# Kernel optimization log

Measured on AMD Instinct MI355X. Metric: run time of the kernel, lower is better.

The kernel has to match this reference:

```python
import jax, jax.numpy as jnp
import numpy as np

N = 20000      # base graph nodes
S = 20         # nodes per subgraph
NC = N * S     # combined subgraph nodes = 400000
EC = 2_000_000 # combined subgraph edges
EB = 200_000   # base graph edges
NIN = 64
HOP = 16
D = NIN + HOP  # 80, conv width
NOUT = 64


def setup_inputs() -> dict:
    key = jax.random.key(0)
    ks = jax.random.split(key, 32)
    f32 = jnp.float32

    batch = jnp.repeat(jnp.arange(N), S)                      # subgraph id per combined node
    offs = jax.random.randint(ks[0], (NC,), 1, N)
    nodes_mapper = (batch + offs) % N                         # never equals batch
    cent_idx = jnp.arange(N) * S
    nodes_mapper = nodes_mapper.at[cent_idx].set(jnp.arange(N))  # exactly one centroid/subgraph

    edge_index = jax.random.randint(ks[1], (2, EC), 0, NC)
    edges_mapper = jax.random.randint(ks[2], (EC,), 0, EB)
    hop_indicator = jax.random.randint(ks[3], (NC,), 0, 19)   # +1 -> [1,19] < 20

    x = jax.random.normal(ks[4], (N, NIN), f32)
    edge_attr = jax.random.normal(ks[5], (EB, D), f32)

    def lin(k, i, o, s=0.05):
        return jax.random.normal(k, (i, o), f32) * s

    inp = dict(
        x=x, edge_attr=edge_attr,
        hop_table=jax.random.normal(ks[6], (20, HOP), f32) * 0.05,
        conv_w1=lin(ks[7], D, D), bn1_g=jnp.ones((D,), f32), bn1_b=jnp.zeros((D,), f32),
        conv_w2=lin(ks[8], D, D), bn2_g=jnp.ones((D,), f32), bn2_b=jnp.zeros((D,), f32),
        oe_w=lin(ks[9], D, NOUT), oe_b=jnp.zeros((NOUT,), f32),
        sub_w=lin(ks[10], NOUT, NOUT), sub_b=jnp.zeros((NOUT,), f32),
        sub_g=jnp.ones((NOUT,), f32), sub_bt=jnp.zeros((NOUT,), f32),
        ctx_w=lin(ks[11], NOUT, NOUT), ctx_b=jnp.zeros((NOUT,), f32),
        ctx_g=jnp.ones((NOUT,), f32), ctx_bt=jnp.zeros((NOUT,), f32),
        gc_w=lin(ks[12], HOP, NOUT), gc_b=jnp.zeros((NOUT,), f32),
        gs_w=lin(ks[13], HOP, NOUT), gs_b=jnp.zeros((NOUT,), f32),
        gx_w=lin(ks[14], HOP, NOUT), gx_b=jnp.zeros((NOUT,), f32),
        fo_w=lin(ks[15], NOUT, NOUT), fo_b=jnp.zeros((NOUT,), f32),
        fo_g=jnp.ones((NOUT,), f32), fo_bt=jnp.zeros((NOUT,), f32),
        nodes_mapper=nodes_mapper, edges_mapper=edges_mapper,
        edge_index=edge_index, batch=batch, hop_indicator=hop_indicator,
    )
    return inp


def reference(x, edge_attr, hop_table,
              conv_w1, bn1_g, bn1_b, conv_w2, bn2_g, bn2_b, oe_w, oe_b,
              sub_w, sub_b, sub_g, sub_bt, ctx_w, ctx_b, ctx_g, ctx_bt,
              gc_w, gc_b, gs_w, gs_b, gx_w, gx_b,
              fo_w, fo_b, fo_g, fo_bt,
              nodes_mapper, edges_mapper, edge_index, batch, hop_indicator):
    hop_emb = hop_table[hop_indicator + 1]                       # [NC, HOP]
    h = jnp.concatenate([x[nodes_mapper], hop_emb], axis=-1)     # [NC, D] gather + concat
    ea = edge_attr[edges_mapper]                                 # [EC, D] gather
    src, dst = edge_index[0], edge_index[1]

    def gine_layer(h, W, g, b):
        # GINEConv (eps=0, no bias): Linear(x_i + sum_j ReLU(x_j + e_ji)), then eval-BN + ReLU
        msg = jax.nn.relu(h[src] + ea)                           # [EC, D]
        agg = jax.ops.segment_sum(msg, dst, num_segments=NC)     # scatter-add
        out = (h + agg) @ W
        return jax.nn.relu(g * out + b)

    prev = h
    h = gine_layer(h, conv_w1, bn1_g, bn1_b) + prev
    prev = h
    h = gine_layer(h, conv_w2, bn2_g, bn2_b) + prev
    comb = h @ oe_w + oe_b                                       # [NC, NOUT] output encoder

    gate_c = jax.nn.sigmoid(hop_emb @ gc_w + gc_b)
    gate_s = jax.nn.sigmoid(hop_emb @ gs_w + gs_b)
    gate_x = jax.nn.sigmoid(hop_emb @ gx_w + gx_b)

    # centroid: exactly one node per subgraph with mapper==batch -> masked segment_sum picks it
    mask = (nodes_mapper == batch).astype(comb.dtype)[:, None]
    centroid = jax.ops.segment_sum(comb * gate_c * mask, batch, num_segments=N)

    sub = jax.nn.relu(sub_g * (comb @ sub_w + sub_b) + sub_bt) * gate_s
    ctx = jax.nn.relu(ctx_g * (comb @ ctx_w + ctx_b) + ctx_bt) * gate_x

    ones = jnp.ones((NC,), comb.dtype)
    cnt_b = jnp.clip(jax.ops.segment_sum(ones, batch, num_segments=N), 1.0)
    cnt_m = jnp.clip(jax.ops.segment_sum(ones, nodes_mapper, num_segments=N), 1.0)
    sub_pool = jax.ops.segment_sum(sub, batch, num_segments=N) / cnt_b[:, None]
    ctx_pool = jax.ops.segment_sum(ctx, nodes_mapper, num_segments=N) / cnt_m[:, None]

    out = centroid + sub_pool + ctx_pool                         # embs_combine_mode='add'
    return fo_g * (out @ fo_w + fo_b) + fo_bt                    # out_encoder: Linear + eval-BN
```

## Files before the change

kernel.cpp:

```cpp
#include <hip/hip_runtime.h>
#include <hip/hip_bf16.h>

#define N_    20000
#define S_    20
#define NC_   400000
#define EC_   2000000
#define EB_   200000
#define NIN_  64
#define HOP_  16
#define D_    80
#define NOUT_ 64
#define NB_   1563
#define NBN_  79

typedef __attribute__((ext_vector_type(8))) short bf16x8;
typedef __attribute__((ext_vector_type(4))) float f32x4;
union FragU { uint4 u; bf16x8 b; };

__device__ __forceinline__ float2 bf2f(unsigned u) {
    float2 r;
    r.x = __uint_as_float(u << 16);
    r.y = __uint_as_float(u & 0xffff0000u);
    return r;
}
__device__ __forceinline__ unsigned f2bf_rne(float f) {
    unsigned u = __float_as_uint(f);
    return (u + 0x7fffu + ((u >> 16) & 1u)) >> 16;
}
__device__ __forceinline__ unsigned pack2(float a, float b) {
    return f2bf_rne(a) | (f2bf_rne(b) << 16);
}

__device__ __forceinline__ void acc4(float* A, uint4 hv, uint4 ev) {
    const unsigned* hp = (const unsigned*)&hv;
    const unsigned* ep = (const unsigned*)&ev;
    #pragma unroll
    for (int j = 0; j < 4; j++) {
        float2 hs = bf2f(hp[j]);
        float2 eq = bf2f(ep[j]);
        A[2 * j]     += fmaxf(hs.x + eq.x, 0.f);
        A[2 * j + 1] += fmaxf(hs.y + eq.y, 0.f);
    }
}
__device__ __forceinline__ void acc4f(float* A, uint4 hv, const float* er, int off) {
    const unsigned* hp = (const unsigned*)&hv;
    #pragma unroll
    for (int j = 0; j < 4; j++) {
        float2 hs = bf2f(hp[j]);
        float2 eq = *(const float2*)(er + 2 * (off + j));
        A[2 * j]     += fmaxf(hs.x + eq.x, 0.f);
        A[2 * j + 1] += fmaxf(hs.y + eq.y, 0.f);
    }
}

__device__ __forceinline__ int blockExclScan(int v, int tid, int* lds, int* total) {
    int lane = tid & 63;
    int w = tid >> 6;
    int x = v;
    #pragma unroll
    for (int off = 1; off < 64; off <<= 1) {
        int y = __shfl_up(x, off, 64);
        if (lane >= off) x += y;
    }
    if (lane == 63) lds[w] = x;
    __syncthreads();
    if (tid == 0) {
        int acc = 0;
        #pragma unroll
        for (int i = 0; i < 4; i++) { int t = lds[i]; lds[4 + i] = acc; acc += t; }
        lds[8] = acc;
    }
    __syncthreads();
    int res = x - v + lds[4 + w];
    *total = lds[8];
    return res;
}

__global__ __launch_bounds__(256) void k_degree(const int* __restrict__ eidx, int* __restrict__ deg) {
    int e = blockIdx.x * 256 + threadIdx.x;
    if (e >= EC_) return;
    atomicAdd(&deg[eidx[EC_ + e]], 1);
}

__global__ __launch_bounds__(256) void k_hist(const int* __restrict__ mapper, int* __restrict__ cnt) {
    int i = blockIdx.x * 256 + threadIdx.x;
    if (i >= NC_) return;
    atomicAdd(&cnt[mapper[i]], 1);
}

__global__ __launch_bounds__(256) void k_bsum(const int* __restrict__ deg, int* __restrict__ bsums, int n) {
    __shared__ int lds[9];
    int i = blockIdx.x * 256 + threadIdx.x;
    int v = (i < n) ? deg[i] : 0;
    int tot;
    blockExclScan(v, threadIdx.x, lds, &tot);
    if (threadIdx.x == 0) bsums[blockIdx.x] = tot;
}

__global__ __launch_bounds__(256) void k_scan_bsums(int* __restrict__ bsums, int nb) {
    __shared__ int lds[9];
    int carry = 0;
    for (int base = 0; base < nb; base += 256) {
        int i = base + threadIdx.x;
        int v = (i < nb) ? bsums[i] : 0;
        int tot;
        int ex = blockExclScan(v, threadIdx.x, lds, &tot);
        if (i < nb) bsums[i] = ex + carry;
        carry += tot;
        __syncthreads();
    }
}

__global__ __launch_bounds__(256) void k_scan_apply(
    int* __restrict__ cursor, int* __restrict__ start, const int* __restrict__ bsums,
    int n, int total)
{
    __shared__ int lds[9];
    int i = blockIdx.x * 256 + threadIdx.x;
    int v = (i < n) ? cursor[i] : 0;
    int tot;
    int ex = blockExclScan(v, threadIdx.x, lds, &tot);
    if (i < n) {
        int s = ex + bsums[blockIdx.x];
        start[i] = s;
        cursor[i] = s;
    }
    if (blockIdx.x == 0 && threadIdx.x == 0) start[n] = total;
}

__global__ __launch_bounds__(256) void k_fill(
    const int* __restrict__ eidx, const int* __restrict__ emap,
    const int* __restrict__ hop,
    int* __restrict__ cursor, int2* __restrict__ e2)
{
    int e = blockIdx.x * 256 + threadIdx.x;
    if (e >= EC_) return;
    int src = eidx[e];
    int dst = eidx[EC_ + e];
    int pk = emap[e] * 32 + (hop[src] + 1);
    int pos = atomicAdd(&cursor[dst], 1);
    e2[pos] = make_int2(src, pk);
}

__global__ __launch_bounds__(256) void k_fill_nodes(
    const int* __restrict__ mapper, int* __restrict__ cursor, int* __restrict__ nidx)
{
    int i = blockIdx.x * 256 + threadIdx.x;
    if (i >= NC_) return;
    int pos = atomicAdd(&cursor[mapper[i]], 1);
    nidx[pos] = i;
}

__global__ __launch_bounds__(256) void k_xb16(unsigned* __restrict__ xb, const float* __restrict__ x) {
    int idx = blockIdx.x * 256 + threadIdx.x;
    if (idx >= N_ * 32) return;
    int row = idx >> 5, p = idx & 31;
    float2 v = *(const float2*)(x + (size_t)row * 64 + 2 * p);
    xb[idx] = pack2(v.x, v.y);
}
__global__ __launch_bounds__(160) void k_htb16(unsigned* __restrict__ htb, const float* __restrict__ ht) {
    int idx = threadIdx.x;
    int row = idx >> 3, p = idx & 7;
    float2 v = *(const float2*)(ht + (size_t)row * 16 + 2 * p);
    htb[idx] = pack2(v.x, v.y);
}

__global__ __launch_bounds__(256) void k_ea16(
    unsigned* __restrict__ eab, const float* __restrict__ ea)
{
    int idx = blockIdx.x * 256 + threadIdx.x;
    if (idx >= EB_ * 40) return;
    int row = idx / 40, t = idx - row * 40;
    float2 v = *(const float2*)(ea + (size_t)row * 80 + 2 * t);
    eab[idx] = pack2(v.x, v.y);
}

__global__ __launch_bounds__(64) void k_gates(
    const float* __restrict__ ht,
    const float* __restrict__ gc_w, const float* __restrict__ gc_b,
    const float* __restrict__ gs_w, const float* __restrict__ gs_b,
    const float* __restrict__ gx_w, const float* __restrict__ gx_b,
    float* __restrict__ gall)
{
    int h = blockIdx.x;
    int d = threadIdx.x;
    const float* htr = ht + h * 16;
    float a = gc_b[d], b = gs_b[d], c = gx_b[d];
    #pragma unroll
    for (int k = 0; k < 16; k++) {
        float hk = htr[k];
        a += hk * gc_w[k * 64 + d];
        b += hk * gs_w[k * 64 + d];
        c += hk * gx_w[k * 64 + d];
    }
    gall[h * 64 + d]            = 1.f / (1.f + __expf(-a));
    gall[(20 + h) * 64 + d]     = 1.f / (1.f + __expf(-b));
    gall[(40 + h) * 64 + d]     = 1.f / (1.f + __expf(-c));
}

template<int L, bool EA16>
__global__ __launch_bounds__(256) void k_gine_f(
    const unsigned* __restrict__ hin,
    const unsigned* __restrict__ xb, const unsigned* __restrict__ htb,
    const int* __restrict__ mapper, const int* __restrict__ hop,
    const unsigned* __restrict__ eab, const float* __restrict__ eaf,
    const int* __restrict__ start, const int2* __restrict__ e2,
    unsigned* __restrict__ outp,
    const float* __restrict__ W, const float* __restrict__ gv, const float* __restrict__ bv)
{
    __shared__ unsigned sWB[5 * 16 * 49];
    int tid = threadIdx.x;
    for (int i = tid; i < 5 * 16 * 49; i += 256) {
        int t = i / 784, r2 = i % 784, cc = r2 / 49, kp = r2 % 49;
        int col = 16 * t + cc;
        sWB[i] = (kp < 40) ? pack2(W[(2 * kp) * D_ + col], W[(2 * kp + 1) * D_ + col]) : 0u;
    }
    __syncthreads();

    int w = tid >> 6;
    int lane = tid & 63;
    int q = lane >> 4;
    int c = lane & 15;
    int base = (blockIdx.x * 4 + w) * 16;
    int node = base + c;
    int off0 = 4 * q, off1 = 16 + 4 * q, off2 = 32 + 4 * q;

    float A0[8] = {0.f, 0.f, 0.f, 0.f, 0.f, 0.f, 0.f, 0.f};
    float A1[8] = {0.f, 0.f, 0.f, 0.f, 0.f, 0.f, 0.f, 0.f};
    float A2[8] = {0.f, 0.f, 0.f, 0.f, 0.f, 0.f, 0.f, 0.f};
    uint4 zz = make_uint4(0u, 0u, 0u, 0u);

    int e = start[node];
    int s1 = start[node + 1];
    while (__any(e < s1)) {
        bool a0 = e < s1;
        bool a1 = (e + 1) < s1;
        int ee0 = max(min(e, s1 - 1), 0);
        int ee1 = max(min(e + 1, s1 - 1), 0);
        int2 ed0 = e2[ee0];
        int2 ed1 = e2[ee1];
        uint4 s00, s01, s02, s10, s11, s12;
        if (L == 1) {
            int m0 = mapper[ed0.x];
            int m1 = mapper[ed1.x];
            const unsigned* x0 = xb + (size_t)m0 * 32;
            const unsigned* x1 = xb + (size_t)m1 * 32;
            s00 = *(const uint4*)(x0 + off0);
            s01 = *(const uint4*)(x0 + off1);
            s02 = (q < 2) ? *(const uint4*)(htb + (ed0.y & 31) * 8 + off0) : zz;
            s10 = *(const uint4*)(x1 + off0);
            s11 = *(const uint4*)(x1 + off1);
            s12 = (q < 2) ? *(const uint4*)(htb + (ed1.y & 31) * 8 + off0) : zz;
        } else {
            const unsigned* h0 = hin + (size_t)ed0.x * 40;
            const unsigned* h1 = hin + (size_t)ed1.x * 40;
            s00 = *(const uint4*)(h0 + off0);
            s01 = *(const uint4*)(h0 + off1);
            s02 = (q < 2) ? *(const uint4*)(h0 + off2) : zz;
            s10 = *(const uint4*)(h1 + off0);
            s11 = *(const uint4*)(h1 + off1);
            s12 = (q < 2) ? *(const uint4*)(h1 + off2) : zz;
        }
        int em0 = ed0.y >> 5, em1 = ed1.y >> 5;
        if (EA16) {
            const unsigned* e0p = eab + (size_t)em0 * 40;
            const unsigned* e1p = eab + (size_t)em1 * 40;
            uint4 q00 = *(const uint4*)(e0p + off0);
            uint4 q01 = *(const uint4*)(e0p + off1);
            uint4 q02 = (q < 2) ? *(const uint4*)(e0p + off2) : zz;
            uint4 q10 = *(const uint4*)(e1p + off0);
            uint4 q11 = *(const uint4*)(e1p + off1);
            uint4 q12 = (q < 2) ? *(const uint4*)(e1p + off2) : zz;
            if (a0) { acc4(A0, s00, q00); acc4(A1, s01, q01); if (q < 2) acc4(A2, s02, q02); }
            if (a1) { acc4(A0, s10, q10); acc4(A1, s11, q11); if (q < 2) acc4(A2, s12, q12); }
        } else {
            const float* e0p = eaf + (size_t)em0 * 80;
            const float* e1p = eaf + (size_t)em1 * 80;
            if (a0) { acc4f(A0, s00, e0p, off0); acc4f(A1, s01, e0p, off1); if (q < 2) acc4f(A2, s02, e0p, off2); }
            if (a1) { acc4f(A0, s10, e1p, off0); acc4f(A1, s11, e1p, off1); if (q < 2) acc4f(A2, s12, e1p, off2); }
        }
        e += 2;
    }

    uint4 h0v, h1v, h2v;
    if (L == 1) {
        int m = mapper[node];
        int hp = hop[node] + 1;
        const unsigned* xr = xb + (size_t)m * 32;
        h0v = *(const uint4*)(xr + off0);
        h1v = *(const uint4*)(xr + off1);
        h2v = (q < 2) ? *(const uint4*)(htb + hp * 8 + off0) : zz;
    } else {
        const unsigned* hr = hin + (size_t)node * 40;
        h0v = *(const uint4*)(hr + off0);
        h1v = *(const uint4*)(hr + off1);
        h2v = (q < 2) ? *(const uint4*)(hr + off2) : zz;
    }

    FragU a0F, a1F, a2F;
    {
        const unsigned* hp0 = (const unsigned*)&h0v;
        const unsigned* hp1 = (const unsigned*)&h1v;
        const unsigned* hp2 = (const unsigned*)&h2v;
        unsigned r0[4], r1[4], r2[4];
        #pragma unroll
        for (int j = 0; j < 4; j++) {
            float2 f0 = bf2f(hp0[j]);
            float2 f1 = bf2f(hp1[j]);
            float2 f2 = bf2f(hp2[j]);
            r0[j] = pack2(A0[2 * j] + f0.x, A0[2 * j + 1] + f0.y);
            r1[j] = pack2(A1[2 * j] + f1.x, A1[2 * j + 1] + f1.y);
            r2[j] = (q < 2) ? pack2(A2[2 * j] + f2.x, A2[2 * j + 1] + f2.y) : 0u;
        }
        a0F.u = make_uint4(r0[0], r0[1], r0[2], r0[3]);
        a1F.u = make_uint4(r1[0], r1[1], r1[2], r1[3]);
        a2F.u = make_uint4(r2[0], r2[1], r2[2], r2[3]);
    }

    f32x4 acc[5];
    #pragma unroll
    for (int t = 0; t < 5; t++) {
        const unsigned* pb = sWB + (t * 16 + c) * 49 + 4 * q;
        FragU b0, b1, b2;
        b0.u = *(const uint4*)(pb);
        b1.u = *(const uint4*)(pb + 16);
        b2.u = *(const uint4*)(pb + 32);
        f32x4 z = {0.f, 0.f, 0.f, 0.f};
        acc[t] = __builtin_amdgcn_mfma_f32_16x16x32_bf16(a0F.b, b0.b, z, 0, 0, 0);
        acc[t] = __builtin_amdgcn_mfma_f32_16x16x32_bf16(a1F.b, b1.b, acc[t], 0, 0, 0);
        acc[t] = __builtin_amdgcn_mfma_f32_16x16x32_bf16(a2F.b, b2.b, acc[t], 0, 0, 0);
    }

    int mm2[4], hp2v[4];
    if (L == 1) {
        #pragma unroll
        for (int r = 0; r < 4; r++) {
            int row = base + 4 * q + r;
            mm2[r] = mapper[row];
            hp2v[r] = hop[row] + 1;
        }
    }
    #pragma unroll
    for (int t = 0; t < 5; t++) {
        int col = 16 * t + c;
        float gc_ = gv[col], bc_ = bv[col];
        #pragma unroll
        for (int r = 0; r < 4; r++) {
            int row = base + 4 * q + r;
            unsigned hu;
            if (L == 1) {
                hu = (t < 4) ? xb[(size_t)mm2[r] * 32 + 8 * t + (c >> 1)]
                             : htb[hp2v[r] * 8 + (c >> 1)];
            } else {
                hu = hin[(size_t)row * 40 + 8 * t + (c >> 1)];
            }
            float2 hf = bf2f(hu);
            float hres = (c & 1) ? hf.y : hf.x;
            float o = fmaxf(gc_ * acc[t][r] + bc_, 0.f) + hres;
            float partner = __shfl_xor(o, 1);
            if (!(c & 1)) outp[(size_t)row * 40 + 8 * t + (c >> 1)] = pack2(o, partner);
        }
    }
}

__global__ __launch_bounds__(256) void k_headm(
    const unsigned* __restrict__ h2u, const int* __restrict__ hop,
    const int* __restrict__ mapper, const float* __restrict__ gall,
    const float* __restrict__ oe_w, const float* __restrict__ oe_b,
    const float* __restrict__ sub_w, const float* __restrict__ sub_b,
    const float* __restrict__ sub_g, const float* __restrict__ sub_bt,
    const float* __restrict__ ctx_w, const float* __restrict__ ctx_b,
    const float* __restrict__ ctx_g, const float* __restrict__ ctx_bt,
    float* __restrict__ cent, float* __restrict__ subp, unsigned* __restrict__ ctxv)
{
    __shared__ unsigned sOE[4 * 16 * 48];
    __shared__ unsigned sSB[4 * 16 * 40];
    __shared__ unsigned sCX[4 * 16 * 40];
    __shared__ float    sT[4][16 * 68];
    int tid = threadIdx.x;
    for (int i = tid; i < 4 * 16 * 48; i += 256) {
        int t = i / (16 * 48), r2 = i % (16 * 48), cc = r2 / 48, kp = r2 % 48;
        int col = 16 * t + cc;
        sOE[i] = (kp < 40) ? pack2(oe_w[(2 * kp) * 64 + col], oe_w[(2 * kp + 1) * 64 + col]) : 0u;
    }
    for (int i = tid; i < 4 * 16 * 40; i += 256) {
        int t = i / (16 * 40), r2 = i % (16 * 40), cc = r2 / 40, kp = r2 % 40;
        int col = 16 * t + cc;
        bool ok = kp < 32;
        sSB[i] = ok ? pack2(sub_w[(2 * kp) * 64 + col], sub_w[(2 * kp + 1) * 64 + col]) : 0u;
        sCX[i] = ok ? pack2(ctx_w[(2 * kp) * 64 + col], ctx_w[(2 * kp + 1) * 64 + col]) : 0u;
    }
    __syncthreads();

    int w = tid >> 6;
    int lane = tid & 63;
    int q = lane >> 4;
    int c = lane & 15;
    int base = (blockIdx.x * 4 + w) * 16;

    const uint4* hrow = (const uint4*)(h2u + (size_t)(base + c) * 40);
    FragU a0, a1, a2;
    a0.u = hrow[q];
    a1.u = hrow[4 + q];
    a2.u = make_uint4(0u, 0u, 0u, 0u);
    if (q < 2) a2.u = hrow[8 + q];

    f32x4 acc[4];
    #pragma unroll
    for (int t = 0; t < 4; t++) {
        const unsigned* pb = sOE + (t * 16 + c) * 48 + 4 * q;
        FragU b0, b1, b2;
        b0.u = *(const uint4*)(pb);
        b1.u = *(const uint4*)(pb + 16);
        b2.u = *(const uint4*)(pb + 32);
        f32x4 z = {0.f, 0.f, 0.f, 0.f};
        acc[t] = __builtin_amdgcn_mfma_f32_16x16x32_bf16(a0.b, b0.b, z, 0, 0, 0);
        acc[t] = __builtin_amdgcn_mfma_f32_16x16x32_bf16(a1.b, b1.b, acc[t], 0, 0, 0);
        acc[t] = __builtin_amdgcn_mfma_f32_16x16x32_bf16(a2.b, b2.b, acc[t], 0, 0, 0);
    }

    int mm[4], hn[4];
    #pragma unroll
    for (int r = 0; r < 4; r++) {
        int node = base + 4 * q + r;
        mm[r] = mapper[node];
        hn[r] = hop[node] + 1;
    }
    int sgA = base / S_;
    int k0 = (sgA + 1) * S_ - base;
    if (k0 > 16) k0 = 16;

    #pragma unroll
    for (int t = 0; t < 4; t++) {
        int col = 16 * t + c;
        float ob = oe_b[col];
        #pragma unroll
        for (int r = 0; r < 4; r++) {
            int row = 4 * q + r;
            float v = acc[t][r] + ob;
            sT[w][row * 68 + col] = v;
            int sg = (row < k0) ? sgA : sgA + 1;
            if (mm[r] == sg) {
                cent[(size_t)sg * 64 + col] = v * gall[hn[r] * 64 + col];
            }
        }
    }

    const float* trp = &sT[w][c * 68 + 8 * q];
    float4 v0 = *(const float4*)(trp);
    float4 v1 = *(const float4*)(trp + 4);
    float4 v2 = *(const float4*)(trp + 32);
    float4 v3 = *(const float4*)(trp + 36);
    FragU ap0, ap1;
    ap0.u = make_uint4(pack2(v0.x, v0.y), pack2(v0.z, v0.w), pack2(v1.x, v1.y), pack2(v1.z, v1.w));
    ap1.u = make_uint4(pack2(v2.x, v2.y), pack2(v2.z, v2.w), pack2(v3.x, v3.y), pack2(v3.z, v3.w));

    f32x4 sa[4], ca[4];
    #pragma unroll
    for (int t = 0; t < 4; t++) {
        const unsigned* ps = sSB + (t * 16 + c) * 40 + 4 * q;
        const unsigned* pc = sCX + (t * 16 + c) * 40 + 4 * q;
        FragU b0, b1, d0, d1;
        b0.u = *(const uint4*)(ps);
        b1.u = *(const uint4*)(ps + 16);
        d0.u = *(const uint4*)(pc);
        d1.u = *(const uint4*)(pc + 16);
        f32x4 z = {0.f, 0.f, 0.f, 0.f};
        sa[t] = __builtin_amdgcn_mfma_f32_16x16x32_bf16(ap0.b, b0.b, z, 0, 0, 0);
        sa[t] = __builtin_amdgcn_mfma_f32_16x16x32_bf16(ap1.b, b1.b, sa[t], 0, 0, 0);
        ca[t] = __builtin_amdgcn_mfma_f32_16x16x32_bf16(ap0.b, d0.b, z, 0, 0, 0);
        ca[t] = __builtin_amdgcn_mfma_f32_16x16x32_bf16(ap1.b, d1.b, ca[t], 0, 0, 0);
    }

    #pragma unroll
    for (int t = 0; t < 4; t++) {
        int col = 16 * t + c;
        float sb = sub_b[col], sgm = sub_g[col], sbt = sub_bt[col];
        float cb = ctx_b[col], cgm = ctx_g[col], cbt = ctx_bt[col];
        float sA = 0.f, sB = 0.f;
        #pragma unroll
        for (int r = 0; r < 4; r++) {
            int row = 4 * q + r;
            float sval = fmaxf(sgm * (sa[t][r] + sb) + sbt, 0.f) * gall[(20 + hn[r]) * 64 + col];
            float cval = fmaxf(cgm * (ca[t][r] + cb) + cbt, 0.f) * gall[(40 + hn[r]) * 64 + col];
            float partner = __shfl_xor(cval, 1);
            if ((c & 1) == 0) {
                ctxv[(size_t)(base + row) * 32 + (col >> 1)] = pack2(cval, partner);
            }
            if (row < k0) sA += sval; else sB += sval;
        }
        sA += __shfl_xor(sA, 16); sA += __shfl_xor(sA, 32);
        sB += __shfl_xor(sB, 16); sB += __shfl_xor(sB, 32);
        if (q == 0) {
            atomicAdd(&subp[(size_t)sgA * 64 + col], sA);
            if (k0 < 16) atomicAdd(&subp[(size_t)(sgA + 1) * 64 + col], sB);
        }
    }
}

__global__ __launch_bounds__(256) void k_ctxpool(
    const unsigned* __restrict__ ctxv, const int* __restrict__ nstart,
    const int* __restrict__ nidx, float* __restrict__ ctxp)
{
    int w = threadIdx.x >> 6, d = threadIdx.x & 63;
    int n = blockIdx.x * 4 + w;
    if (n >= N_) return;
    int s0 = nstart[n], s1 = nstart[n + 1];
    int dh = d >> 1;
    float acc = 0.f;
    int i = s0;
    for (; i + 4 <= s1; i += 4) {
        int r0 = nidx[i], r1 = nidx[i + 1], r2 = nidx[i + 2], r3 = nidx[i + 3];
        float2 f0 = bf2f(ctxv[(size_t)r0 * 32 + dh]);
        float2 f1 = bf2f(ctxv[(size_t)r1 * 32 + dh]);
        float2 f2 = bf2f(ctxv[(size_t)r2 * 32 + dh]);
        float2 f3 = bf2f(ctxv[(size_t)r3 * 32 + dh]);
        acc += (d & 1) ? (f0.y + f1.y + f2.y + f3.y) : (f0.x + f1.x + f2.x + f3.x);
    }
    for (; i < s1; i++) {
        float2 f = bf2f(ctxv[(size_t)nidx[i] * 32 + dh]);
        acc += (d & 1) ? f.y : f.x;
    }
    ctxp[(size_t)n * 64 + d] = acc;
}

__global__ __launch_bounds__(256) void k_final(
    const float* __restrict__ cent, const float* __restrict__ subp, const float* __restrict__ ctxp,
    const int* __restrict__ nstart,
    const float* __restrict__ fo_w, const float* __restrict__ fo_b,
    const float* __restrict__ fo_g, const float* __restrict__ fo_bt,
    float* __restrict__ out)
{
    __shared__ float sW[64 * 64];
    int tid = threadIdx.x;
    for (int i = tid; i < 4096; i += 256) sW[i] = fo_w[i];
    int d = tid & 63, grp = tid >> 6;
    float rb = fo_b[d], rg = fo_g[d], rbt = fo_bt[d];
    __syncthreads();
    for (int n = blockIdx.x * 4 + grp; n < N_; n += gridDim.x * 4) {
        float cm = (float)max(nstart[n + 1] - nstart[n], 1);
        size_t o = (size_t)n * 64 + d;
        float r = cent[o] + subp[o] * (1.f / 20.f) + ctxp[o] / cm;
        float dot = rb;
        #pragma unroll 8
        for (int k = 0; k < 64; k++) dot += __shfl(r, k) * sW[k * 64 + d];
        out[o] = rg * dot + rbt;
    }
}

extern "C" void kernel_launch(void* const* d_in, const int* in_sizes, int n_in,
                              void* d_out, int out_size, void* d_ws, size_t ws_size,
                              hipStream_t stream) {
    const float* x         = (const float*)d_in[0];
    const float* edge_attr = (const float*)d_in[1];
    const float* hop_table = (const float*)d_in[2];
    const float* conv_w1   = (const float*)d_in[3];
    const float* bn1_g     = (const float*)d_in[4];
    const float* bn1_b     = (const float*)d_in[5];
    const float* conv_w2   = (const float*)d_in[6];
    const float* bn2_g     = (const float*)d_in[7];
    const float* bn2_b     = (const float*)d_in[8];
    const float* oe_w      = (const float*)d_in[9];
    const float* oe_b      = (const float*)d_in[10];
    const float* sub_w     = (const float*)d_in[11];
    const float* sub_b     = (const float*)d_in[12];
    const float* sub_g     = (const float*)d_in[13];
    const float* sub_bt    = (const float*)d_in[14];
    const float* ctx_w     = (const float*)d_in[15];
    const float* ctx_b     = (const float*)d_in[16];
    const float* ctx_g     = (const float*)d_in[17];
    const float* ctx_bt    = (const float*)d_in[18];
    const float* gc_w      = (const float*)d_in[19];
    const float* gc_b      = (const float*)d_in[20];
    const float* gs_w      = (const float*)d_in[21];
    const float* gs_b      = (const float*)d_in[22];
    const float* gx_w      = (const float*)d_in[23];
    const float* gx_b      = (const float*)d_in[24];
    const float* fo_w      = (const float*)d_in[25];
    const float* fo_b      = (const float*)d_in[26];
    const float* fo_g      = (const float*)d_in[27];
    const float* fo_bt     = (const float*)d_in[28];
    const int* nodes_mapper  = (const int*)d_in[29];
    const int* edges_mapper  = (const int*)d_in[30];
    const int* edge_index    = (const int*)d_in[31];
    const int* batch         = (const int*)d_in[32];
    const int* hop_indicator = (const int*)d_in[33];
    (void)batch;
    float* out = (float*)d_out;

    size_t off = 0;
    auto alloc = [&](size_t bytes) -> char* {
        char* p = (char*)d_ws + off;
        off = (off + bytes + 255) & ~(size_t)255;
        return p;
    };
    unsigned* hbuf0 = (unsigned*)alloc((size_t)NC_ * 40 * 4);
    unsigned* hbuf1 = (unsigned*)alloc((size_t)NC_ * 40 * 4);
    int*   start    = (int*)alloc((size_t)(NC_ + 1) * 4);
    int*   cursor   = (int*)alloc((size_t)NC_ * 4);
    int*   bsums    = (int*)alloc(2048 * 4);
    int2*  e2       = (int2*)alloc((size_t)EC_ * 8);
    float* cent     = (float*)alloc((size_t)N_ * 64 * 4);
    float* subp     = (float*)alloc((size_t)N_ * 64 * 4);
    float* ctxp     = (float*)alloc((size_t)N_ * 64 * 4);
    int*   nstart   = (int*)alloc((size_t)(N_ + 1) * 4);
    int*   cursor_n = (int*)alloc((size_t)N_ * 4);
    int*   bsums_n  = (int*)alloc(256 * 4);
    int*   nidx     = (int*)alloc((size_t)NC_ * 4);
    float* gall     = (float*)alloc((size_t)60 * 64 * 4);
    unsigned* xb    = (unsigned*)alloc((size_t)N_ * 32 * 4);
    unsigned* htb   = (unsigned*)alloc((size_t)20 * 8 * 4);
    size_t ea16_bytes = (size_t)EB_ * 40 * 4;
    bool use_ea16 = (off + ea16_bytes + 256) <= ws_size;
    unsigned* eab = use_ea16 ? (unsigned*)alloc(ea16_bytes) : nullptr;
    unsigned* ctxv = hbuf1;
    (void)in_sizes; (void)n_in; (void)out_size;

    hipMemsetAsync(cursor, 0, (size_t)NC_ * 4, stream);
    hipMemsetAsync(cursor_n, 0, (size_t)N_ * 4, stream);
    hipMemsetAsync(subp, 0, (size_t)N_ * 64 * 4, stream);

    k_xb16<<<(N_ * 32 + 255) / 256, 256, 0, stream>>>(xb, x);
    k_htb16<<<1, 160, 0, stream>>>(htb, hop_table);
    k_gates<<<20, 64, 0, stream>>>(hop_table, gc_w, gc_b, gs_w, gs_b, gx_w, gx_b, gall);
    if (use_ea16)
        k_ea16<<<(EB_ * 40 + 255) / 256, 256, 0, stream>>>(eab, edge_attr);

    k_degree<<<(EC_ + 255) / 256, 256, 0, stream>>>(edge_index, cursor);
    k_bsum<<<NB_, 256, 0, stream>>>(cursor, bsums, NC_);
    k_scan_bsums<<<1, 256, 0, stream>>>(bsums, NB_);
    k_scan_apply<<<NB_, 256, 0, stream>>>(cursor, start, bsums, NC_, EC_);
    k_fill<<<(EC_ + 255) / 256, 256, 0, stream>>>(edge_index, edges_mapper, hop_indicator,
                                                  cursor, e2);

    k_hist<<<(NC_ + 255) / 256, 256, 0, stream>>>(nodes_mapper, cursor_n);
    k_bsum<<<NBN_, 256, 0, stream>>>(cursor_n, bsums_n, N_);
    k_scan_bsums<<<1, 256, 0, stream>>>(bsums_n, NBN_);
    k_scan_apply<<<NBN_, 256, 0, stream>>>(cursor_n, nstart, bsums_n, N_, NC_);
    k_fill_nodes<<<(NC_ + 255) / 256, 256, 0, stream>>>(nodes_mapper, cursor_n, nidx);

    if (use_ea16) {
        k_gine_f<1, true><<<NC_ / 64, 256, 0, stream>>>(nullptr, xb, htb, nodes_mapper,
                                                        hop_indicator, eab, edge_attr,
                                                        start, e2, hbuf1, conv_w1, bn1_g, bn1_b);
        k_gine_f<2, true><<<NC_ / 64, 256, 0, stream>>>(hbuf1, xb, htb, nodes_mapper,
                                                        hop_indicator, eab, edge_attr,
                                                        start, e2, hbuf0, conv_w2, bn2_g, bn2_b);
    } else {
        k_gine_f<1, false><<<NC_ / 64, 256, 0, stream>>>(nullptr, xb, htb, nodes_mapper,
                                                         hop_indicator, eab, edge_attr,
                                                         start, e2, hbuf1, conv_w1, bn1_g, bn1_b);
        k_gine_f<2, false><<<NC_ / 64, 256, 0, stream>>>(hbuf1, xb, htb, nodes_mapper,
                                                         hop_indicator, eab, edge_attr,
                                                         start, e2, hbuf0, conv_w2, bn2_g, bn2_b);
    }

    k_headm<<<NC_ / 64, 256, 0, stream>>>(hbuf0, hop_indicator, nodes_mapper, gall,
                                          oe_w, oe_b, sub_w, sub_b, sub_g, sub_bt,
                                          ctx_w, ctx_b, ctx_g, ctx_bt,
                                          cent, subp, ctxv);

    k_ctxpool<<<N_ / 4, 256, 0, stream>>>(ctxv, nstart, nidx, ctxp);

    k_final<<<1280, 256, 0, stream>>>(cent, subp, ctxp, nstart, fo_w, fo_b, fo_g, fo_bt, out);
}
```

Baseline: 1.118 ms.

## Sort nodes by in-degree so each wavefront processes similar-degree nodes

Adds a degree histogram, scan and scatter pass that builds a permutation of nodes ordered by in-degree. The two GINE conv kernels then assign nodes to lanes through this permutation, so the 16 nodes sharing a wavefront's edge loop have similar degree and the __any loop wastes fewer iterations on idle lanes. This costs three extra small kernels with atomics, plus an extra indirection and scattered output writes, since consecutive rows in a tile no longer map to consecutive memory.

```diff
diff --git a/kernel.cpp b/kernel.cpp
--- a/kernel.cpp
+++ b/kernel.cpp
@@ -12,6 +12,7 @@
 #define NOUT_ 64
 #define NB_   1563
 #define NBN_  79
+#define DBIN_ 64
 
 typedef __attribute__((ext_vector_type(8))) short bf16x8;
 typedef __attribute__((ext_vector_type(4))) float f32x4;
@@ -151,6 +152,33 @@
     nidx[pos] = i;
 }
 
+__global__ __launch_bounds__(256) void k_dhist(const int* __restrict__ start, int* __restrict__ dhist) {
+    int i = blockIdx.x * 256 + threadIdx.x;
+    if (i >= NC_) return;
+    int d = min(start[i + 1] - start[i], DBIN_ - 1);
+    atomicAdd(&dhist[d], 1);
+}
+__global__ __launch_bounds__(64) void k_dscan(const int* __restrict__ dhist, int* __restrict__ dcur) {
+    int lane = threadIdx.x;
+    int v = dhist[lane];
+    int x = v;
+    #pragma unroll
+    for (int off = 1; off < 64; off <<= 1) {
+        int y = __shfl_up(x, off, 64);
+        if (lane >= off) x += y;
+    }
+    dcur[lane] = x - v;
+}
+__global__ __launch_bounds__(256) void k_dscatter(
+    const int* __restrict__ start, int* __restrict__ dcur, int* __restrict__ porder)
+{
+    int i = blockIdx.x * 256 + threadIdx.x;
+    if (i >= NC_) return;
+    int d = min(start[i + 1] - start[i], DBIN_ - 1);
+    int pos = atomicAdd(&dcur[d], 1);
+    porder[pos] = i;
+}
+
 __global__ __launch_bounds__(256) void k_xb16(unsigned* __restrict__ xb, const float* __restrict__ x) {
     int idx = blockIdx.x * 256 + threadIdx.x;
     if (idx >= N_ * 32) return;
@@ -205,6 +233,7 @@
     const int* __restrict__ mapper, const int* __restrict__ hop,
     const unsigned* __restrict__ eab, const float* __restrict__ eaf,
     const int* __restrict__ start, const int2* __restrict__ e2,
+    const int* __restrict__ porder,
     unsigned* __restrict__ outp,
     const float* __restrict__ W, const float* __restrict__ gv, const float* __restrict__ bv)
 {
@@ -222,7 +251,7 @@
     int q = lane >> 4;
     int c = lane & 15;
     int base = (blockIdx.x * 4 + w) * 16;
-    int node = base + c;
+    int node = porder[base + c];
     int off0 = 4 * q, off1 = 16 + 4 * q, off2 = 32 + 4 * q;
 
     float A0[8] = {0.f, 0.f, 0.f, 0.f, 0.f, 0.f, 0.f, 0.f};
@@ -331,13 +360,13 @@
         acc[t] = __builtin_amdgcn_mfma_f32_16x16x32_bf16(a2F.b, b2.b, acc[t], 0, 0, 0);
     }
 
-    int mm2[4], hp2v[4];
-    if (L == 1) {
-        #pragma unroll
-        for (int r = 0; r < 4; r++) {
-            int row = base + 4 * q + r;
-            mm2[r] = mapper[row];
-            hp2v[r] = hop[row] + 1;
+    int prow[4], mm2[4], hp2v[4];
+    #pragma unroll
+    for (int r = 0; r < 4; r++) {
+        prow[r] = porder[base + 4 * q + r];
+        if (L == 1) {
+            mm2[r] = mapper[prow[r]];
+            hp2v[r] = hop[prow[r]] + 1;
         }
     }
     #pragma unroll
@@ -346,19 +375,18 @@
         float gc_ = gv[col], bc_ = bv[col];
         #pragma unroll
         for (int r = 0; r < 4; r++) {
-            int row = base + 4 * q + r;
             unsigned hu;
             if (L == 1) {
                 hu = (t < 4) ? xb[(size_t)mm2[r] * 32 + 8 * t + (c >> 1)]
                              : htb[hp2v[r] * 8 + (c >> 1)];
             } else {
-                hu = hin[(size_t)row * 40 + 8 * t + (c >> 1)];
+                hu = hin[(size_t)prow[r] * 40 + 8 * t + (c >> 1)];
             }
             float2 hf = bf2f(hu);
             float hres = (c & 1) ? hf.y : hf.x;
             float o = fmaxf(gc_ * acc[t][r] + bc_, 0.f) + hres;
             float partner = __shfl_xor(o, 1);
-            if (!(c & 1)) outp[(size_t)row * 40 + 8 * t + (c >> 1)] = pack2(o, partner);
+            if (!(c & 1)) outp[(size_t)prow[r] * 40 + 8 * t + (c >> 1)] = pack2(o, partner);
         }
     }
 }
@@ -610,6 +638,9 @@
     float* gall     = (float*)alloc((size_t)60 * 64 * 4);
     unsigned* xb    = (unsigned*)alloc((size_t)N_ * 32 * 4);
     unsigned* htb   = (unsigned*)alloc((size_t)20 * 8 * 4);
+    int*   dhist    = (int*)alloc(DBIN_ * 4);
+    int*   dcur     = (int*)alloc(DBIN_ * 4);
+    int*   porder   = (int*)alloc((size_t)NC_ * 4);
     size_t ea16_bytes = (size_t)EB_ * 40 * 4;
     bool use_ea16 = (off + ea16_bytes + 256) <= ws_size;
     unsigned* eab = use_ea16 ? (unsigned*)alloc(ea16_bytes) : nullptr;
@@ -619,6 +650,7 @@
     hipMemsetAsync(cursor, 0, (size_t)NC_ * 4, stream);
     hipMemsetAsync(cursor_n, 0, (size_t)N_ * 4, stream);
     hipMemsetAsync(subp, 0, (size_t)N_ * 64 * 4, stream);
+    hipMemsetAsync(dhist, 0, DBIN_ * 4, stream);
 
     k_xb16<<<(N_ * 32 + 255) / 256, 256, 0, stream>>>(xb, x);
     k_htb16<<<1, 160, 0, stream>>>(htb, hop_table);
@@ -633,6 +665,10 @@
     k_fill<<<(EC_ + 255) / 256, 256, 0, stream>>>(edge_index, edges_mapper, hop_indicator,
                                                   cursor, e2);
 
+    k_dhist<<<(NC_ + 255) / 256, 256, 0, stream>>>(start, dhist);
+    k_dscan<<<1, 64, 0, stream>>>(dhist, dcur);
+    k_dscatter<<<(NC_ + 255) / 256, 256, 0, stream>>>(start, dcur, porder);
+
     k_hist<<<(NC_ + 255) / 256, 256, 0, stream>>>(nodes_mapper, cursor_n);
     k_bsum<<<NBN_, 256, 0, stream>>>(cursor_n, bsums_n, N_);
     k_scan_bsums<<<1, 256, 0, stream>>>(bsums_n, NBN_);
@@ -642,17 +678,21 @@
     if (use_ea16) {
         k_gine_f<1, true><<<NC_ / 64, 256, 0, stream>>>(nullptr, xb, htb, nodes_mapper,
                                                         hop_indicator, eab, edge_attr,
-                                                        start, e2, hbuf1, conv_w1, bn1_g, bn1_b);
+                                                        start, e2, porder, hbuf1,
+                                                        conv_w1, bn1_g, bn1_b);
         k_gine_f<2, true><<<NC_ / 64, 256, 0, stream>>>(hbuf1, xb, htb, nodes_mapper,
                                                         hop_indicator, eab, edge_attr,
-                                                        start, e2, hbuf0, conv_w2, bn2_g, bn2_b);
+                                                        start, e2, porder, hbuf0,
+                                                        conv_w2, bn2_g, bn2_b);
     } else {
         k_gine_f<1, false><<<NC_ / 64, 256, 0, stream>>>(nullptr, xb, htb, nodes_mapper,
                                                          hop_indicator, eab, edge_attr,
-                                                         start, e2, hbuf1, conv_w1, bn1_g, bn1_b);
+                                                         start, e2, porder, hbuf1,
+                                                         conv_w1, bn1_g, bn1_b);
         k_gine_f<2, false><<<NC_ / 64, 256, 0, stream>>>(hbuf1, xb, htb, nodes_mapper,
                                                          hop_indicator, eab, edge_attr,
-                                                         start, e2, hbuf0, conv_w2, bn2_g, bn2_b);
+                                                         start, e2, porder, hbuf0,
+                                                         conv_w2, bn2_g, bn2_b);
     }
 
     k_headm<<<NC_ / 64, 256, 0, stream>>>(hbuf0, hop_indicator, nodes_mapper, gall,
```

Measured after the change: 4.126 ms. 3.69x slower.
